# Kernel optimization log

Hardware: AMD Instinct MI355X
Metric: run time of the kernel (lower is better)

Reference implementation:

```python
import jax, jax.numpy as jnp
import numpy as np

B, N, D = 1, 4096, 512
H, DH, M, WIN = 8, 64, 4, 512
QK_SCALE = 10.0  # qk_norm_scale


def _l2norm(t):
    # F.normalize(p=2, dim=-1) with groups=1
    n = jnp.linalg.norm(t, axis=-1, keepdims=True)
    return t / jnp.maximum(n, 1e-12)


def _rotate_half(t):
    t1, t2 = jnp.split(t, 2, axis=-1)
    return jnp.concatenate([-t2, t1], axis=-1)


def setup_inputs() -> dict:
    key = jax.random.key(0)
    ks = jax.random.split(key, 9)
    s = 0.02
    x = jax.random.normal(ks[0], (B, N, D), jnp.float32)
    Wq = jax.random.normal(ks[1], (D, H * DH), jnp.float32) * s
    Wk = jax.random.normal(ks[2], (D, H * DH), jnp.float32) * s
    Wv = jax.random.normal(ks[3], (D, H * DH), jnp.float32) * s
    Wg = jax.random.normal(ks[4], (D, H * DH), jnp.float32) * s
    bg = jnp.ones((H * DH,), jnp.float32)  # torch init: bias=1
    Wo = jax.random.normal(ks[5], (H * DH, D), jnp.float32) * s
    mem_k = jax.random.normal(ks[6], (H, M, DH), jnp.float32)
    mem_v = jax.random.normal(ks[7], (H, M, DH), jnp.float32)
    # standard rotary table, duplicated halves so rotate_half pairing matches
    half = DH // 2
    inv = 1.0 / (10000.0 ** (np.arange(half, dtype=np.float32) / half))
    f = np.outer(np.arange(N, dtype=np.float32), inv)  # [N, DH/2]
    freqs = jnp.asarray(np.concatenate([f, f], axis=-1), jnp.float32)  # [N, DH]
    return {"x": x, "Wq": Wq, "Wk": Wk, "Wv": Wv, "Wg": Wg, "bg": bg,
            "Wo": Wo, "mem_k": mem_k, "mem_v": mem_v, "freqs": freqs}


def reference(x, Wq, Wk, Wv, Wg, bg, Wo, mem_k, mem_v, freqs):
    # projections -> b h n d
    def split_heads(t):
        return t.reshape(B, N, H, DH).transpose(0, 2, 1, 3)
    q = split_heads(x @ Wq)
    k = split_heads(x @ Wk)
    v = split_heads(x @ Wv)
    # qk-norm (groups=1), scale handled via QK_SCALE later
    q = _l2norm(q)
    k = _l2norm(k)
    # rotary (l == DH so full head dim is rotated)
    cos = jnp.cos(freqs)  # [N, DH]
    sin = jnp.sin(freqs)
    q = q * cos + _rotate_half(q) * sin
    k = k * cos + _rotate_half(k) * sin
    # memory KV concat (mem_k goes through l2norm under qk_norm)
    mk = jnp.broadcast_to(_l2norm(mem_k)[None], (B, H, M, DH))
    mv = jnp.broadcast_to(mem_v[None], (B, H, M, DH))
    k = jnp.concatenate([mk, k], axis=2)  # [B,H,M+N,DH]
    v = jnp.concatenate([mv, v], axis=2)
    J = N + M
    # local window mask: queries at positions M..J-1, keys at 0..J-1
    rq = jnp.arange(M, J)
    rk = jnp.arange(J)
    dist = rq[:, None] - rk[None, :]
    allowed = (dist <= WIN) & (dist >= -WIN)  # [N, J]
    sim = jnp.einsum('bhid,bhjd->bhij', q, k) * QK_SCALE
    neg = -jnp.finfo(sim.dtype).max
    sim = jnp.where(allowed[None, None], sim, neg)
    attn = jax.nn.softmax(sim, axis=-1)
    out = jnp.einsum('bhij,bhjd->bhid', attn, v)  # [B,H,N,DH]
    out = out.transpose(0, 2, 1, 3).reshape(B, N, H * DH)
    # value gating
    gates = x @ Wg + bg
    out = out * jax.nn.sigmoid(gates)
    return out @ Wo
```

## Files before the change

### kernel.cpp

```cpp
#include <hip/hip_runtime.h>
#include <math.h>

#define TN 4096
#define DM 512
#define NH 8
#define DHD 64
#define MEM 4
#define WINR 512
#define JTOT (TN + MEM)
#define JPAD 4168
#define QK_SCALE 10.0f

typedef __attribute__((ext_vector_type(8))) short bf16x8;
typedef __attribute__((ext_vector_type(4))) float f32x4;

__device__ __forceinline__ unsigned short f2bf(float f) {
    unsigned u = __float_as_uint(f);
    u = (u + 0x7FFFu + ((u >> 16) & 1u)) >> 16;
    return (unsigned short)u;
}

__device__ __forceinline__ void gl_lds16(const unsigned short* g, unsigned short* l) {
    __builtin_amdgcn_global_load_lds(
        (const __attribute__((address_space(1))) unsigned int*)g,
        (__attribute__((address_space(3))) unsigned int*)l, 16, 0, 0);
}

__global__ __launch_bounds__(256)
void prep(const float* __restrict__ X, unsigned short* __restrict__ Xb,
          const float* __restrict__ W0, const float* __restrict__ W1,
          const float* __restrict__ W2, const float* __restrict__ W3,
          const float* __restrict__ W4, unsigned short* __restrict__ T,
          const float* __restrict__ freqs, float2* __restrict__ tab,
          const float* __restrict__ mem_k, const float* __restrict__ mem_v,
          unsigned short* __restrict__ k_b, unsigned short* __restrict__ v_b)
{
    const int b = blockIdx.x;
    const int t = threadIdx.x;

    if (b < 2048) {
        int idx = b * 256 + t;
        float4 v = *(const float4*)&X[(size_t)idx * 4];
        *(ushort4*)&Xb[(size_t)idx * 4] =
            make_ushort4(f2bf(v.x), f2bf(v.y), f2bf(v.z), f2bf(v.w));
    } else if (b < 2368) {
        __shared__ unsigned short Ts[64][68];
        int bi = b - 2048;
        int sel = bi >> 6, tile = bi & 63;
        const float* __restrict__ W =
            (sel == 0) ? W0 : (sel == 1) ? W1 : (sel == 2) ? W2 : (sel == 3) ? W3 : W4;
        unsigned short* __restrict__ Wt = T + (size_t)sel * DM * DM;
        int r0 = (tile >> 3) * 64, c0 = (tile & 7) * 64;
        #pragma unroll
        for (int p = 0; p < 4; ++p) {
            int i  = p * 16 + (t >> 4);
            int j4 = (t & 15) * 4;
            float4 v = *(const float4*)&W[(size_t)(r0 + i) * DM + c0 + j4];
            Ts[i][j4 + 0] = f2bf(v.x); Ts[i][j4 + 1] = f2bf(v.y);
            Ts[i][j4 + 2] = f2bf(v.z); Ts[i][j4 + 3] = f2bf(v.w);
        }
        __syncthreads();
        #pragma unroll
        for (int p = 0; p < 4; ++p) {
            int oc  = p * 16 + (t >> 4);
            int or4 = (t & 15) * 4;
            *(ushort4*)&Wt[(size_t)(c0 + oc) * DM + r0 + or4] =
                make_ushort4(Ts[or4 + 0][oc], Ts[or4 + 1][oc],
                             Ts[or4 + 2][oc], Ts[or4 + 3][oc]);
        }
    } else if (b < 2432) {
        int tid = (b - 2368) * 256 + t;
        #pragma unroll
        for (int e = 0; e < 16; ++e) {
            int id = e * 16384 + tid;
            float f = freqs[id];
            float sn, cs;
            sincosf(f, &sn, &cs);
            tab[id] = make_float2(cs, sn);
        }
    } else {
        int gw   = (b - 2432) * 4 + (t >> 6);
        int lane = t & 63;
        int h = gw >> 2, m = gw & 3;
        float kv = mem_k[(size_t)(h * MEM + m) * DHD + lane];
        float s = kv * kv;
        #pragma unroll
        for (int off = 1; off < 64; off <<= 1) s += __shfl_xor(s, off);
        kv = kv / fmaxf(sqrtf(s), 1e-12f);
        k_b[((size_t)h * JPAD + m) * 64 + lane] = f2bf(kv);
        v_b[((size_t)h * JPAD + m) * 64 + lane] =
            f2bf(mem_v[(size_t)(h * MEM + m) * DHD + lane]);
    }
}

__global__ __launch_bounds__(256)
void gemm_qkvg_mfma(const unsigned short* __restrict__ Xb,
                    const unsigned short* __restrict__ Wt,
                    const float2* __restrict__ tab,
                    const float* __restrict__ bg,
                    unsigned short* __restrict__ q_b,
                    unsigned short* __restrict__ k_b,
                    unsigned short* __restrict__ v_b,
                    float* __restrict__ graw)
{
    __shared__ __align__(16) unsigned short As[128][32];
    __shared__ __align__(16) unsigned short Bs[128][32];
    const int sel = blockIdx.z;
    const unsigned short* __restrict__ Wsel = Wt + (size_t)sel * DM * DM;
    const int row0 = blockIdx.x * 128;
    const int col0 = blockIdx.y * 128;
    const int t = threadIdx.x;
    const int w = t >> 6, l = t & 63;
    const int wm = w >> 1, wn = w & 1;
    const int l15 = l & 15, lh = l >> 4;
    const int wb = t & 192;

    f32x4 acc[4][4];
    #pragma unroll
    for (int mi = 0; mi < 4; ++mi)
        #pragma unroll
        for (int ni = 0; ni < 4; ++ni)
            acc[mi][ni] = (f32x4){0.f, 0.f, 0.f, 0.f};

    for (int k0 = 0; k0 < DM; k0 += 32) {
        __syncthreads();
        #pragma unroll
        for (int cc = 0; cc < 2; ++cc) {
            int c = t + cc * 256;
            int row = c >> 2, k8 = c & 3;
            gl_lds16(&Xb[(size_t)(row0 + row) * DM + k0 + k8 * 8],
                     &As[0][0] + (size_t)(wb + cc * 256) * 8);
            gl_lds16(&Wsel[(size_t)(col0 + row) * DM + k0 + k8 * 8],
                     &Bs[0][0] + (size_t)(wb + cc * 256) * 8);
        }
        __syncthreads();

        bf16x8 af[4], bfr[4];
        #pragma unroll
        for (int mi = 0; mi < 4; ++mi)
            af[mi] = *(const bf16x8*)&As[wm * 64 + mi * 16 + l15][lh * 8];
        #pragma unroll
        for (int ni = 0; ni < 4; ++ni)
            bfr[ni] = *(const bf16x8*)&Bs[wn * 64 + ni * 16 + l15][lh * 8];
        #pragma unroll
        for (int mi = 0; mi < 4; ++mi)
            #pragma unroll
            for (int ni = 0; ni < 4; ++ni)
                acc[mi][ni] = __builtin_amdgcn_mfma_f32_16x16x32_bf16(
                    af[mi], bfr[ni], acc[mi][ni], 0, 0, 0);
    }

    if (sel <= 1) {
        const int h = (col0 + wn * 64) >> 6;
        #pragma unroll
        for (int mi = 0; mi < 4; ++mi) {
            #pragma unroll
            for (int r = 0; r < 4; ++r) {
                float v0 = acc[mi][0][r], v1 = acc[mi][1][r];
                float v2 = acc[mi][2][r], v3 = acc[mi][3][r];
                float ss = v0 * v0 + v1 * v1 + v2 * v2 + v3 * v3;
                ss += __shfl_xor(ss, 1); ss += __shfl_xor(ss, 2);
                ss += __shfl_xor(ss, 4); ss += __shfl_xor(ss, 8);
                float inv = 1.0f / fmaxf(sqrtf(ss), 1e-12f);
                v0 *= inv; v1 *= inv; v2 *= inv; v3 *= inv;
                int n = row0 + wm * 64 + mi * 16 + lh * 4 + r;
                float2 t0 = tab[n * 64 + l15];
                float2 t1 = tab[n * 64 + 16 + l15];
                float o0 = v0 * t0.x - v2 * t0.y;
                float o1 = v1 * t1.x - v3 * t1.y;
                float o2 = v2 * t0.x + v0 * t0.y;
                float o3 = v3 * t1.x + v1 * t1.y;
                unsigned short* dst = (sel == 0)
                    ? &q_b[((size_t)h * TN + n) * 64]
                    : &k_b[((size_t)h * JPAD + MEM + n) * 64];
                dst[l15]      = f2bf(o0);
                dst[16 + l15] = f2bf(o1);
                dst[32 + l15] = f2bf(o2);
                dst[48 + l15] = f2bf(o3);
            }
        }
    } else if (sel == 2) {
        const int h = (col0 + wn * 64) >> 6;
        #pragma unroll
        for (int mi = 0; mi < 4; ++mi)
            #pragma unroll
            for (int ni = 0; ni < 4; ++ni) {
                int d = ni * 16 + l15;
                #pragma unroll
                for (int r = 0; r < 4; ++r) {
                    int grow = row0 + wm * 64 + mi * 16 + lh * 4 + r;
                    v_b[((size_t)h * JPAD + MEM + grow) * 64 + d] = f2bf(acc[mi][ni][r]);
                }
            }
    } else {
        #pragma unroll
        for (int mi = 0; mi < 4; ++mi)
            #pragma unroll
            for (int ni = 0; ni < 4; ++ni) {
                int gcol = col0 + wn * 64 + ni * 16 + l15;
                float bgv = bg[gcol];
                #pragma unroll
                for (int r = 0; r < 4; ++r) {
                    int grow = row0 + wm * 64 + mi * 16 + lh * 4 + r;
                    float g = acc[mi][ni][r] + bgv;
                    graw[(size_t)grow * DM + gcol] = 1.0f / (1.0f + __expf(-g));
                }
            }
    }
}

__global__ __launch_bounds__(256)
void gemm_out_mfma(const unsigned short* __restrict__ Ab,
                   const unsigned short* __restrict__ Wot,
                   float* __restrict__ C)
{
    __shared__ __align__(16) unsigned short As[128][32];
    __shared__ __align__(16) unsigned short Bs[128][32];
    const int row0 = blockIdx.x * 128;
    const int col0 = blockIdx.y * 128;
    const int t = threadIdx.x;
    const int w = t >> 6, l = t & 63;
    const int wm = w >> 1, wn = w & 1;
    const int wb = t & 192;

    f32x4 acc[4][4];
    #pragma unroll
    for (int mi = 0; mi < 4; ++mi)
        #pragma unroll
        for (int ni = 0; ni < 4; ++ni)
            acc[mi][ni] = (f32x4){0.f, 0.f, 0.f, 0.f};

    for (int k0 = 0; k0 < DM; k0 += 32) {
        __syncthreads();
        #pragma unroll
        for (int cc = 0; cc < 2; ++cc) {
            int c = t + cc * 256;
            int row = c >> 2, k8 = c & 3;
            gl_lds16(&Ab[(size_t)(row0 + row) * DM + k0 + k8 * 8],
                     &As[0][0] + (size_t)(wb + cc * 256) * 8);
            gl_lds16(&Wot[(size_t)(col0 + row) * DM + k0 + k8 * 8],
                     &Bs[0][0] + (size_t)(wb + cc * 256) * 8);
        }
        __syncthreads();

        bf16x8 af[4], bfr[4];
        #pragma unroll
        for (int mi = 0; mi < 4; ++mi)
            af[mi] = *(const bf16x8*)&As[wm * 64 + mi * 16 + (l & 15)][(l >> 4) * 8];
        #pragma unroll
        for (int ni = 0; ni < 4; ++ni)
            bfr[ni] = *(const bf16x8*)&Bs[wn * 64 + ni * 16 + (l & 15)][(l >> 4) * 8];
        #pragma unroll
        for (int mi = 0; mi < 4; ++mi)
            #pragma unroll
            for (int ni = 0; ni < 4; ++ni)
                acc[mi][ni] = __builtin_amdgcn_mfma_f32_16x16x32_bf16(
                    af[mi], bfr[ni], acc[mi][ni], 0, 0, 0);
    }

    #pragma unroll
    for (int mi = 0; mi < 4; ++mi)
        #pragma unroll
        for (int ni = 0; ni < 4; ++ni) {
            int gcol = col0 + wn * 64 + ni * 16 + (l & 15);
            #pragma unroll
            for (int r = 0; r < 4; ++r) {
                int grow = row0 + wm * 64 + mi * 16 + (l >> 4) * 4 + r;
                C[(size_t)grow * DM + gcol] = acc[mi][ni][r];
            }
        }
}

#define TILE_US (64 * 72)
__global__ __launch_bounds__(512)
void attn_mfma(const unsigned short* __restrict__ qb,
               const unsigned short* __restrict__ kb,
               const unsigned short* __restrict__ vb,
               const float* __restrict__ gate,
               unsigned short* __restrict__ attnb)
{
    __shared__ __align__(16) unsigned short smem[TILE_US * 7];
    unsigned short* Qs = smem;
    #define KS(g) (smem + TILE_US * (1 + (g)))
    #define VT(g) (smem + TILE_US * (3 + (g)))
    #define PS(g) (smem + TILE_US * (5 + (g)))

    const int sw   = (blockIdx.x & 7) * 64 + (blockIdx.x >> 3);
    const int head = sw >> 6;
    const int n0   = (sw & 63) * 64;
    const int t   = threadIdx.x;
    const int g   = t >> 8;
    const int tig = t & 255;
    const int wid = (t >> 6) & 3;
    const int l   = t & 63;
    const int l15 = l & 15, lh = l >> 4;

    {
        int row = t >> 3, c8 = (t & 7) * 8;
        *(bf16x8*)&Qs[row * 72 + c8] =
            *(const bf16x8*)&qb[((size_t)(head * TN + n0 + row)) * 64 + c8];
    }

    f32x4 oacc[4];
    #pragma unroll
    for (int dt = 0; dt < 4; ++dt) oacc[dt] = (f32x4){0.f, 0.f, 0.f, 0.f};
    float lpart[4] = {0.f, 0.f, 0.f, 0.f};

    const int p_base = MEM + n0;
    const int kstart = max(0, p_base - WINR);
    const int kend   = min(JTOT, p_base + 63 + WINR + 1);
    const int ntiles = (kend - kstart + 63) >> 6;
    const int niter  = (ntiles + 1) >> 1;

    const int srow = tig >> 3, sc8 = (tig & 7) * 8;
    const int srow2 = (tig + 256) >> 3, sc82 = ((tig + 256) & 7) * 8;
    const int vj = tig & 63, vd0 = (tig >> 6) * 8;
    const int vj2 = (tig + 256) & 63, vd02 = ((tig + 256) >> 6) * 8;
    bf16x8 kr0, kr1, vr0, vr1;

    int tj = g;
    {
        int j0 = kstart + tj * 64;
        kr0 = *(const bf16x8*)&kb[((size_t)head * JPAD + j0 + srow) * 64 + sc8];
        kr1 = *(const bf16x8*)&kb[((size_t)head * JPAD + j0 + srow2) * 64 + sc82];
        vr0 = *(const bf16x8*)&vb[((size_t)head * JPAD + j0 + vj) * 64 + vd0];
        vr1 = *(const bf16x8*)&vb[((size_t)head * JPAD + j0 + vj2) * 64 + vd02];
    }

    for (int it = 0; it < niter; ++it) {
        bool valid = (tj < ntiles);
        __syncthreads();
        if (valid) {
            *(bf16x8*)&KS(g)[srow * 72 + sc8]   = kr0;
            *(bf16x8*)&KS(g)[srow2 * 72 + sc82] = kr1;
            #pragma unroll
            for (int i = 0; i < 8; ++i) VT(g)[(vd0 + i) * 72 + vj]   = (unsigned short)vr0[i];
            #pragma unroll
            for (int i = 0; i < 8; ++i) VT(g)[(vd02 + i) * 72 + vj2] = (unsigned short)vr1[i];
        }
        __syncthreads();

        if (valid) {
            int j0 = kstart + tj * 64;
            if (tj + 2 < ntiles) {
                int jn = kstart + (tj + 2) * 64;
                kr0 = *(const bf16x8*)&kb[((size_t)head * JPAD + jn + srow) * 64 + sc8];
                kr1 = *(const bf16x8*)&kb[((size_t)head * JPAD + jn + srow2) * 64 + sc82];
                vr0 = *(const bf16x8*)&vb[((size_t)head * JPAD + jn + vj) * 64 + vd0];
                vr1 = *(const bf16x8*)&vb[((size_t)head * JPAD + jn + vj2) * 64 + vd02];
            }

            f32x4 sacc[4];
            #pragma unroll
            for (int kt = 0; kt < 4; ++kt) sacc[kt] = (f32x4){0.f, 0.f, 0.f, 0.f};
            __builtin_amdgcn_s_setprio(1);
            #pragma unroll
            for (int s = 0; s < 2; ++s) {
                bf16x8 a = *(const bf16x8*)&Qs[(wid * 16 + l15) * 72 + s * 32 + lh * 8];
                #pragma unroll
                for (int kt = 0; kt < 4; ++kt) {
                    bf16x8 b = *(const bf16x8*)&KS(g)[(kt * 16 + l15) * 72 + s * 32 + lh * 8];
                    sacc[kt] = __builtin_amdgcn_mfma_f32_16x16x32_bf16(a, b, sacc[kt], 0, 0, 0);
                }
            }
            __builtin_amdgcn_s_setprio(0);

            int qlo = p_base + wid * 16;
            bool fullok = ((qlo + 15 - j0) <= WINR) &&
                          ((qlo - (j0 + 63)) >= -WINR) &&
                          (j0 + 63 < JTOT);
            if (fullok) {
                #pragma unroll
                for (int r = 0; r < 4; ++r) {
                    #pragma unroll
                    for (int kt = 0; kt < 4; ++kt) {
                        float pe = __expf(sacc[kt][r] * QK_SCALE - 10.0f);
                        lpart[r] += pe;
                        PS(g)[(wid * 16 + lh * 4 + r) * 72 + kt * 16 + l15] = f2bf(pe);
                    }
                }
            } else {
                #pragma unroll
                for (int r = 0; r < 4; ++r) {
                    int pq = p_base + wid * 16 + lh * 4 + r;
                    #pragma unroll
                    for (int kt = 0; kt < 4; ++kt) {
                        int j = j0 + kt * 16 + l15;
                        int dist = pq - j;
                        bool ok = (dist <= WINR) && (dist >= -WINR) && (j < JTOT);
                        float pe = ok ? __expf(sacc[kt][r] * QK_SCALE - 10.0f) : 0.f;
                        lpart[r] += pe;
                        PS(g)[(wid * 16 + lh * 4 + r) * 72 + kt * 16 + l15] = f2bf(pe);
                    }
                }
            }

            __builtin_amdgcn_s_setprio(1);
            #pragma unroll
            for (int s = 0; s < 2; ++s) {
                bf16x8 a = *(const bf16x8*)&PS(g)[(wid * 16 + l15) * 72 + s * 32 + lh * 8];
                #pragma unroll
                for (int dt = 0; dt < 4; ++dt) {
                    bf16x8 b = *(const bf16x8*)&VT(g)[(dt * 16 + l15) * 72 + s * 32 + lh * 8];
                    oacc[dt] = __builtin_amdgcn_mfma_f32_16x16x32_bf16(a, b, oacc[dt], 0, 0, 0);
                }
            }
            __builtin_amdgcn_s_setprio(0);
        }
        tj += 2;
    }

    float* fbuf = (float*)smem;
    __syncthreads();
    if (g == 1) {
        #pragma unroll
        for (int dt = 0; dt < 4; ++dt)
            #pragma unroll
            for (int r = 0; r < 4; ++r)
                fbuf[tig * 21 + dt * 4 + r] = oacc[dt][r];
        #pragma unroll
        for (int r = 0; r < 4; ++r) fbuf[tig * 21 + 16 + r] = lpart[r];
    }
    __syncthreads();
    if (g == 0) {
        #pragma unroll
        for (int dt = 0; dt < 4; ++dt)
            #pragma unroll
            for (int r = 0; r < 4; ++r)
                oacc[dt][r] += fbuf[tig * 21 + dt * 4 + r];
        #pragma unroll
        for (int r = 0; r < 4; ++r) lpart[r] += fbuf[tig * 21 + 16 + r];

        #pragma unroll
        for (int r = 0; r < 4; ++r) {
            float rs = lpart[r];
            rs += __shfl_xor(rs, 1); rs += __shfl_xor(rs, 2);
            rs += __shfl_xor(rs, 4); rs += __shfl_xor(rs, 8);
            float inv = 1.0f / rs;
            int n = n0 + wid * 16 + lh * 4 + r;
            #pragma unroll
            for (int dt = 0; dt < 4; ++dt) {
                int col = head * 64 + dt * 16 + l15;
                float gv = gate[(size_t)n * DM + col];
                attnb[(size_t)n * DM + col] = f2bf(oacc[dt][r] * inv * gv);
            }
        }
    }
}

extern "C" void kernel_launch(void* const* d_in, const int* in_sizes, int n_in,
                              void* d_out, int out_size, void* d_ws, size_t ws_size,
                              hipStream_t stream)
{
    const float* x     = (const float*)d_in[0];
    const float* Wq    = (const float*)d_in[1];
    const float* Wk    = (const float*)d_in[2];
    const float* Wv    = (const float*)d_in[3];
    const float* Wg    = (const float*)d_in[4];
    const float* bg    = (const float*)d_in[5];
    const float* Wo    = (const float*)d_in[6];
    const float* mem_k = (const float*)d_in[7];
    const float* mem_v = (const float*)d_in[8];
    const float* freqs = (const float*)d_in[9];

    unsigned short* q_b = (unsigned short*)d_ws;
    unsigned short* k_b = q_b + (size_t)NH * TN * DHD;
    unsigned short* v_b = k_b + (size_t)NH * JPAD * DHD;
    unsigned short* Xb  = v_b + (size_t)NH * JPAD * DHD;
    unsigned short* attnb = Xb;
    unsigned short* Wt  = Xb + (size_t)TN * DM;
    float* graw = (float*)(Wt + (size_t)5 * DM * DM);
    float2* tab = (float2*)(graw + (size_t)TN * DM);

    prep<<<dim3(2440), 256, 0, stream>>>(x, Xb, Wq, Wk, Wv, Wg, Wo, Wt,
                                         freqs, tab, mem_k, mem_v, k_b, v_b);

    gemm_qkvg_mfma<<<dim3(TN / 128, DM / 128, 4), 256, 0, stream>>>(
        Xb, Wt, tab, bg, q_b, k_b, v_b, graw);

    attn_mfma<<<dim3(512), 512, 0, stream>>>(q_b, k_b, v_b, graw, attnb);

    gemm_out_mfma<<<dim3(TN / 128, DM / 128), 256, 0, stream>>>(
        attnb, Wt + (size_t)4 * DM * DM, (float*)d_out);
}
```

Before: 143.5 us.

## Split attention key tiles across three wave groups and keep Q in registers

The attention kernel now uses 768 threads, so three groups of four waves each take every third key/value tile instead of two groups taking every other one. The combine step sums partial outputs and row sums from two groups instead of one. The Q tile is loaded straight into registers instead of staged in LDS, and the LDS row pitch shrinks from 72 to 68 to fit nine tiles. This aims at more parallel work per block and lower LDS use, but risks more bank conflicts from the new pitch, fewer resident blocks per CU, and extra reduction cost.

```diff
diff --git a/kernel.cpp b/kernel.cpp
--- a/kernel.cpp
+++ b/kernel.cpp
@@ -271,19 +271,18 @@
         }
 }
 
-#define TILE_US (64 * 72)
-__global__ __launch_bounds__(512)
+#define TILE68 (64 * 68)
+__global__ __launch_bounds__(768)
 void attn_mfma(const unsigned short* __restrict__ qb,
                const unsigned short* __restrict__ kb,
                const unsigned short* __restrict__ vb,
                const float* __restrict__ gate,
                unsigned short* __restrict__ attnb)
 {
-    __shared__ __align__(16) unsigned short smem[TILE_US * 7];
-    unsigned short* Qs = smem;
-    #define KS(g) (smem + TILE_US * (1 + (g)))
-    #define VT(g) (smem + TILE_US * (3 + (g)))
-    #define PS(g) (smem + TILE_US * (5 + (g)))
+    __shared__ __align__(16) unsigned short smem[TILE68 * 9];
+    #define KS(g) (smem + TILE68 * (g))
+    #define VT(g) (smem + TILE68 * (3 + (g)))
+    #define PS(g) (smem + TILE68 * (6 + (g)))
 
     const int sw   = (blockIdx.x & 7) * 64 + (blockIdx.x >> 3);
     const int head = sw >> 6;
@@ -291,15 +290,15 @@
     const int t   = threadIdx.x;
     const int g   = t >> 8;
     const int tig = t & 255;
-    const int wid = (t >> 6) & 3;
+    const int wid = (tig >> 6);
     const int l   = t & 63;
     const int l15 = l & 15, lh = l >> 4;
 
-    {
-        int row = t >> 3, c8 = (t & 7) * 8;
-        *(bf16x8*)&Qs[row * 72 + c8] =
-            *(const bf16x8*)&qb[((size_t)(head * TN + n0 + row)) * 64 + c8];
-    }
+    bf16x8 qr[2];
+    #pragma unroll
+    for (int s = 0; s < 2; ++s)
+        qr[s] = *(const bf16x8*)&qb[((size_t)(head * TN + n0 + wid * 16 + l15)) * 64
+                                    + s * 32 + lh * 8];
 
     f32x4 oacc[4];
     #pragma unroll
@@ -310,7 +309,7 @@
     const int kstart = max(0, p_base - WINR);
     const int kend   = min(JTOT, p_base + 63 + WINR + 1);
     const int ntiles = (kend - kstart + 63) >> 6;
-    const int niter  = (ntiles + 1) >> 1;
+    const int niter  = (ntiles + 2) / 3;
 
     const int srow = tig >> 3, sc8 = (tig & 7) * 8;
     const int srow2 = (tig + 256) >> 3, sc82 = ((tig + 256) & 7) * 8;
@@ -331,19 +330,19 @@
         bool valid = (tj < ntiles);
         __syncthreads();
         if (valid) {
-            *(bf16x8*)&KS(g)[srow * 72 + sc8]   = kr0;
-            *(bf16x8*)&KS(g)[srow2 * 72 + sc82] = kr1;
-            #pragma unroll
-            for (int i = 0; i < 8; ++i) VT(g)[(vd0 + i) * 72 + vj]   = (unsigned short)vr0[i];
-            #pragma unroll
-            for (int i = 0; i < 8; ++i) VT(g)[(vd02 + i) * 72 + vj2] = (unsigned short)vr1[i];
+            *(bf16x8*)&KS(g)[srow * 68 + sc8]   = kr0;
+            *(bf16x8*)&KS(g)[srow2 * 68 + sc82] = kr1;
+            #pragma unroll
+            for (int i = 0; i < 8; ++i) VT(g)[(vd0 + i) * 68 + vj]   = (unsigned short)vr0[i];
+            #pragma unroll
+            for (int i = 0; i < 8; ++i) VT(g)[(vd02 + i) * 68 + vj2] = (unsigned short)vr1[i];
         }
         __syncthreads();
 
         if (valid) {
             int j0 = kstart + tj * 64;
-            if (tj + 2 < ntiles) {
-                int jn = kstart + (tj + 2) * 64;
+            if (tj + 3 < ntiles) {
+                int jn = kstart + (tj + 3) * 64;
                 kr0 = *(const bf16x8*)&kb[((size_t)head * JPAD + jn + srow) * 64 + sc8];
                 kr1 = *(const bf16x8*)&kb[((size_t)head * JPAD + jn + srow2) * 64 + sc82];
                 vr0 = *(const bf16x8*)&vb[((size_t)head * JPAD + jn + vj) * 64 + vd0];
@@ -356,11 +355,10 @@
             __builtin_amdgcn_s_setprio(1);
             #pragma unroll
             for (int s = 0; s < 2; ++s) {
-                bf16x8 a = *(const bf16x8*)&Qs[(wid * 16 + l15) * 72 + s * 32 + lh * 8];
                 #pragma unroll
                 for (int kt = 0; kt < 4; ++kt) {
-                    bf16x8 b = *(const bf16x8*)&KS(g)[(kt * 16 + l15) * 72 + s * 32 + lh * 8];
-                    sacc[kt] = __builtin_amdgcn_mfma_f32_16x16x32_bf16(a, b, sacc[kt], 0, 0, 0);
+                    bf16x8 b = *(const bf16x8*)&KS(g)[(kt * 16 + l15) * 68 + s * 32 + lh * 8];
+                    sacc[kt] = __builtin_amdgcn_mfma_f32_16x16x32_bf16(qr[s], b, sacc[kt], 0, 0, 0);
                 }
             }
             __builtin_amdgcn_s_setprio(0);
@@ -376,7 +374,7 @@
                     for (int kt = 0; kt < 4; ++kt) {
                         float pe = __expf(sacc[kt][r] * QK_SCALE - 10.0f);
                         lpart[r] += pe;
-                        PS(g)[(wid * 16 + lh * 4 + r) * 72 + kt * 16 + l15] = f2bf(pe);
+                        PS(g)[(wid * 16 + lh * 4 + r) * 68 + kt * 16 + l15] = f2bf(pe);
                     }
                 }
             } else {
@@ -390,7 +388,7 @@
                         bool ok = (dist <= WINR) && (dist >= -WINR) && (j < JTOT);
                         float pe = ok ? __expf(sacc[kt][r] * QK_SCALE - 10.0f) : 0.f;
                         lpart[r] += pe;
-                        PS(g)[(wid * 16 + lh * 4 + r) * 72 + kt * 16 + l15] = f2bf(pe);
+                        PS(g)[(wid * 16 + lh * 4 + r) * 68 + kt * 16 + l15] = f2bf(pe);
                     }
                 }
             }
@@ -398,38 +396,43 @@
             __builtin_amdgcn_s_setprio(1);
             #pragma unroll
             for (int s = 0; s < 2; ++s) {
-                bf16x8 a = *(const bf16x8*)&PS(g)[(wid * 16 + l15) * 72 + s * 32 + lh * 8];
+                bf16x8 a = *(const bf16x8*)&PS(g)[(wid * 16 + l15) * 68 + s * 32 + lh * 8];
                 #pragma unroll
                 for (int dt = 0; dt < 4; ++dt) {
-                    bf16x8 b = *(const bf16x8*)&VT(g)[(dt * 16 + l15) * 72 + s * 32 + lh * 8];
+                    bf16x8 b = *(const bf16x8*)&VT(g)[(dt * 16 + l15) * 68 + s * 32 + lh * 8];
                     oacc[dt] = __builtin_amdgcn_mfma_f32_16x16x32_bf16(a, b, oacc[dt], 0, 0, 0);
                 }
             }
             __builtin_amdgcn_s_setprio(0);
         }
-        tj += 2;
+        tj += 3;
     }
 
     float* fbuf = (float*)smem;
     __syncthreads();
-    if (g == 1) {
+    if (g >= 1) {
+        int base = (g - 1) * 256 * 21 + tig * 21;
         #pragma unroll
         for (int dt = 0; dt < 4; ++dt)
             #pragma unroll
             for (int r = 0; r < 4; ++r)
-                fbuf[tig * 21 + dt * 4 + r] = oacc[dt][r];
-        #pragma unroll
-        for (int r = 0; r < 4; ++r) fbuf[tig * 21 + 16 + r] = lpart[r];
+                fbuf[base + dt * 4 + r] = oacc[dt][r];
+        #pragma unroll
+        for (int r = 0; r < 4; ++r) fbuf[base + 16 + r] = lpart[r];
     }
     __syncthreads();
     if (g == 0) {
         #pragma unroll
-        for (int dt = 0; dt < 4; ++dt)
-            #pragma unroll
-            for (int r = 0; r < 4; ++r)
-                oacc[dt][r] += fbuf[tig * 21 + dt * 4 + r];
-        #pragma unroll
-        for (int r = 0; r < 4; ++r) lpart[r] += fbuf[tig * 21 + 16 + r];
+        for (int gg = 0; gg < 2; ++gg) {
+            int base = gg * 256 * 21 + tig * 21;
+            #pragma unroll
+            for (int dt = 0; dt < 4; ++dt)
+                #pragma unroll
+                for (int r = 0; r < 4; ++r)
+                    oacc[dt][r] += fbuf[base + dt * 4 + r];
+            #pragma unroll
+            for (int r = 0; r < 4; ++r) lpart[r] += fbuf[base + 16 + r];
+        }
 
         #pragma unroll
         for (int r = 0; r < 4; ++r) {
@@ -478,7 +481,7 @@
     gemm_qkvg_mfma<<<dim3(TN / 128, DM / 128, 4), 256, 0, stream>>>(
         Xb, Wt, tab, bg, q_b, k_b, v_b, graw);
 
-    attn_mfma<<<dim3(512), 512, 0, stream>>>(q_b, k_b, v_b, graw, attnb);
+    attn_mfma<<<dim3(512), 768, 0, stream>>>(q_b, k_b, v_b, graw, attnb);
 
     gemm_out_mfma<<<dim3(TN / 128, DM / 128), 256, 0, stream>>>(
         attnb, Wt + (size_t)4 * DM * DM, (float*)d_out);
```

Result: no change. 146.1 us (+1.8%).
